# Performance work log

Measured on AMD Instinct MI355X. Metric: run time of the kernel, lower is better.

The kernel has to match this reference:

```python
import jax, jax.numpy as jnp
import numpy as np

T = 3          # num_node_type
B = 8          # batch
N = 512        # max_doc_len
F_IN = 256     # in_features
F_OUT = 128    # out_features
NE = 10        # num_edge_type (embedding has NE+1 rows, row 0 = padding)
ALPHA = 0.2    # leaky relu slope
NEG = -9e15    # masked-score fill, same constant as torch source


def setup_inputs() -> dict:
    key = jax.random.key(0)
    ks = jax.random.split(key, 7)
    node_rep = jax.random.normal(ks[0], (B, N, F_IN), jnp.float32)
    node_type_mask_rep = jax.random.uniform(ks[1], (T, B, N, 1), jnp.float32)
    adj = jax.random.randint(ks[2], (B, N, N), 0, NE + 1, jnp.int32)
    W = jax.random.normal(ks[3], (T, F_IN, F_OUT), jnp.float32) * 0.05
    b = jnp.zeros((T, F_OUT), jnp.float32)
    # attention vector a in R^{2F} split into halves (GAT trick): a([h_i, x2_ij]) = h_i.a1 + x2_ij.a2 + a_b
    a1 = jax.random.normal(ks[4], (F_OUT,), jnp.float32) * 0.05
    a2 = jax.random.normal(ks[5], (F_OUT,), jnp.float32) * 0.05
    a_b = jnp.zeros((), jnp.float32)
    emb = jax.random.normal(ks[6], (NE + 1, F_OUT), jnp.float32) * 0.05
    emb = emb.at[0].set(0.0)  # padding_idx=0
    return {"node_rep": node_rep, "node_type_mask_rep": node_type_mask_rep,
            "adj": adj, "W": W, "b": b, "a1": a1, "a2": a2, "a_b": a_b, "emb": emb}


def reference(node_rep, node_type_mask_rep, adj, W, b, a1, a2, a_b, emb):
    # typed projection: h = sum_t (node_rep @ W_t + b_t) * mask_t   -> (B, N, F_OUT)
    h = jnp.sum((jnp.einsum('bni,tio->tbno', node_rep, W) + b[:, None, None, :])
                * node_type_mask_rep, axis=0)
    # edge-type embeddings: (B, N, N, F_OUT)
    E = emb[adj]
    # x_2[b,i,j] = h[b,j] + E[b,i,j]
    x2 = h[:, None, :, :] + E
    # score[b,i,j] = leakyrelu(a1.h_i + a2.x2_ij + a_b)  (decomposed concat-linear)
    s = (jnp.einsum('bif,f->bi', h, a1)[:, :, None]
         + jnp.einsum('bijf,f->bij', x2, a2) + a_b)
    s = jnp.where(s > 0, s, ALPHA * s)
    s = jnp.where(adj > 0, s, jnp.float32(NEG))
    attn = jax.nn.softmax(s, axis=2)
    # weighted sum over neighbors of x_2 (NOT h), then ELU
    out = jnp.einsum('bij,bijf->bif', attn, x2)
    return jax.nn.elu(out)
```

## Files before the change

### kernel.cpp

```cpp
#include <hip/hip_runtime.h>

constexpr int kB    = 8;
constexpr int kN    = 512;
constexpr int kFIN  = 256;
constexpr int kFOUT = 128;
constexpr int kNE   = 10;
constexpr int kBN   = kB * kN;
constexpr float kALPHA = 0.2f;
constexpr float kNEG   = -9e15f;

typedef __attribute__((ext_vector_type(8))) short bhalf8;
typedef __attribute__((ext_vector_type(4))) float f32x4;

__device__ __forceinline__ unsigned short bf16_trunc(float x) {
    union { float f; unsigned u; } c; c.f = x;
    return (unsigned short)(c.u >> 16);
}
__device__ __forceinline__ float bf16_tof(unsigned short h) {
    union { unsigned u; float f; } c; c.u = ((unsigned)h) << 16;
    return c.f;
}

__global__ __launch_bounds__(256) void prep_kernel(
    const float* __restrict__ W,
    const float* __restrict__ emb,
    const float* __restrict__ a2,
    unsigned short* __restrict__ Whp,
    unsigned short* __restrict__ Wlp,
    float* __restrict__ emb_a2)
{
    const int tid = threadIdx.x;
    if (blockIdx.x < 48) {
        const int g    = blockIdx.x * 256 + tid;
        const int lane = g & 63;
        const int nt   = (g >> 6) & 7;
        const int ks   = (g >> 9) & 7;
        const int tt   = g >> 12;
        const int col  = nt * 16 + (lane & 15);
        const int kb   = ks * 32 + ((lane >> 4) * 8);
        unsigned short hbuf[8], lbuf[8];
        #pragma unroll
        for (int j = 0; j < 8; ++j) {
            const float w = W[((size_t)tt * kFIN + kb + j) * kFOUT + col];
            hbuf[j] = bf16_trunc(w);
            lbuf[j] = bf16_trunc(w - bf16_tof(hbuf[j]));
        }
        const size_t dst = ((size_t)((tt * 8 + ks) * 8 + nt)) * 512 + lane * 8;
        #pragma unroll
        for (int j = 0; j < 8; ++j) { Whp[dst + j] = hbuf[j]; Wlp[dst + j] = lbuf[j]; }
    } else if (tid < 176) {
        const int e = tid >> 4, l = tid & 15;
        float p = 0.f;
        #pragma unroll
        for (int k8 = 0; k8 < 8; ++k8)
            p += emb[e * kFOUT + l + k8 * 16] * a2[l + k8 * 16];
        #pragma unroll
        for (int off = 8; off; off >>= 1) p += __shfl_xor(p, off);
        if (l == 0) emb_a2[e] = p;
    }
}

__global__ __launch_bounds__(512) void proj_kernel(
    const float* __restrict__ node_rep,
    const float* __restrict__ mask,
    const float* __restrict__ bias,
    const unsigned short* __restrict__ Whp,
    const unsigned short* __restrict__ Wlp,
    const float* __restrict__ a1,
    const float* __restrict__ a2,
    const float* __restrict__ a_b,
    float* __restrict__ h,
    float* __restrict__ s1,
    float* __restrict__ s2)
{
    __shared__ short xsh[32][264];
    __shared__ short xsl[32][264];

    const int tid  = threadIdx.x;
    const int row0 = blockIdx.x * 32;

    #pragma unroll
    for (int it = 0; it < 4; ++it) {
        const int idx = tid + it * 512;
        const int r = idx >> 6, q = idx & 63;
        const float4 v = *(const float4*)&node_rep[(size_t)(row0 + r) * kFIN + q * 4];
        ushort4 hi, lo;
        hi.x = bf16_trunc(v.x); lo.x = bf16_trunc(v.x - bf16_tof(hi.x));
        hi.y = bf16_trunc(v.y); lo.y = bf16_trunc(v.y - bf16_tof(hi.y));
        hi.z = bf16_trunc(v.z); lo.z = bf16_trunc(v.z - bf16_tof(hi.z));
        hi.w = bf16_trunc(v.w); lo.w = bf16_trunc(v.w - bf16_tof(hi.w));
        *(ushort4*)&xsh[r][q * 4] = hi;
        *(ushort4*)&xsl[r][q * 4] = lo;
    }
    __syncthreads();

    const int wave = tid >> 6, lane = tid & 63;
    const int wrow = wave & 1, wcol = wave >> 1;
    const int arow = wrow * 16 + (lane & 15);
    const int koff = (lane >> 4) * 8;

    f32x4 acc[3][2];
    #pragma unroll
    for (int t = 0; t < 3; ++t)
        #pragma unroll
        for (int nt = 0; nt < 2; ++nt) acc[t][nt] = (f32x4){0,0,0,0};

    #pragma unroll 2
    for (int ks = 0; ks < 8; ++ks) {
        const bhalf8 Ah = *(const bhalf8*)&xsh[arow][ks * 32 + koff];
        const bhalf8 Al = *(const bhalf8*)&xsl[arow][ks * 32 + koff];
        #pragma unroll
        for (int t = 0; t < 3; ++t)
            #pragma unroll
            for (int nt = 0; nt < 2; ++nt) {
                const size_t bw =
                    ((size_t)((t * 8 + ks) * 8 + wcol * 2 + nt)) * 512 + lane * 8;
                const bhalf8 Bh = *(const bhalf8*)(Whp + bw);
                const bhalf8 Bl = *(const bhalf8*)(Wlp + bw);
                acc[t][nt] = __builtin_amdgcn_mfma_f32_16x16x32_bf16(Ah, Bh, acc[t][nt], 0, 0, 0);
                acc[t][nt] = __builtin_amdgcn_mfma_f32_16x16x32_bf16(Ah, Bl, acc[t][nt], 0, 0, 0);
                acc[t][nt] = __builtin_amdgcn_mfma_f32_16x16x32_bf16(Al, Bh, acc[t][nt], 0, 0, 0);
            }
    }
    __syncthreads();

    float* hstash = (float*)xsh;

    const int rA = wrow * 16 + ((lane >> 4) * 4);
    const int cA = lane & 15;
    #pragma unroll
    for (int j = 0; j < 4; ++j) {
        const int row = row0 + rA + j;
        const float m0 = mask[row];
        const float m1 = mask[kBN + row];
        const float m2 = mask[2 * kBN + row];
        #pragma unroll
        for (int nt = 0; nt < 2; ++nt) {
            const int col = wcol * 32 + nt * 16 + cA;
            const float hv = m0 * (acc[0][nt][j] + bias[col])
                           + m1 * (acc[1][nt][j] + bias[kFOUT + col])
                           + m2 * (acc[2][nt][j] + bias[2 * kFOUT + col]);
            h[(size_t)row * kFOUT + col] = hv;
            hstash[(rA + j) * 132 + col] = hv;
        }
    }
    __syncthreads();

    #pragma unroll
    for (int rr = 0; rr < 4; ++rr) {
        const int r = wave * 4 + rr;
        const float v0 = hstash[r * 132 + lane];
        const float v1 = hstash[r * 132 + 64 + lane];
        float p1 = v0 * a1[lane] + v1 * a1[64 + lane];
        float p2 = v0 * a2[lane] + v1 * a2[64 + lane];
        #pragma unroll
        for (int off = 32; off; off >>= 1) {
            p1 += __shfl_down(p1, off);
            p2 += __shfl_down(p2, off);
        }
        if (lane == 0) {
            s1[row0 + r] = p1 + a_b[0];
            s2[row0 + r] = p2;
        }
    }
}

__global__ __launch_bounds__(512) void attn_kernel(
    const int*   __restrict__ adj,
    const float* __restrict__ emb,
    const float* __restrict__ h,
    const float* __restrict__ s1,
    const float* __restrict__ s2,
    const float* __restrict__ emb_a2g,
    float* __restrict__ out)
{
    __shared__ float sc[8][kN + 4];
    __shared__ int   adjs[8][kN];
    __shared__ float scT[kN][8];
    __shared__ float wsum[8][16];
    __shared__ float ea2[16];

    const int tid = threadIdx.x;
    const int b   = blockIdx.x >> 6;
    const int i0  = (blockIdx.x & 63) * 8;

    if (tid < 16) ea2[tid] = emb_a2g[tid];
    __syncthreads();

    const int*   adjb = adj + ((size_t)(b * kN + i0)) * kN;
    const float* s2b  = s2 + b * kN;
    #pragma unroll
    for (int it = 0; it < 2; ++it) {
        const int idx = tid + it * 512;
        const int r = idx >> 7, jq = idx & 127;
        const int4   av  = *(const int4*)&adjb[(size_t)r * kN + jq * 4];
        const float4 s2v = *(const float4*)&s2b[jq * 4];
        const float  sr  = s1[b * kN + i0 + r];
        float4 sv; float s;
        s = sr + s2v.x + ea2[av.x]; s = s > 0.f ? s : kALPHA * s; sv.x = av.x > 0 ? s : kNEG;
        s = sr + s2v.y + ea2[av.y]; s = s > 0.f ? s : kALPHA * s; sv.y = av.y > 0 ? s : kNEG;
        s = sr + s2v.z + ea2[av.z]; s = s > 0.f ? s : kALPHA * s; sv.z = av.z > 0 ? s : kNEG;
        s = sr + s2v.w + ea2[av.w]; s = s > 0.f ? s : kALPHA * s; sv.w = av.w > 0 ? s : kNEG;
        *(float4*)&sc[r][jq * 4] = sv;
        *(int4*)&adjs[r][jq * 4] = av;
    }
    __syncthreads();

    {
        const int r = tid >> 6, lane = tid & 63;
        float v[8]; int av[8];
        #pragma unroll
        for (int k = 0; k < 8; ++k) {
            v[k]  = sc[r][lane + k * 64];
            av[k] = adjs[r][lane + k * 64];
        }
        float m = v[0];
        #pragma unroll
        for (int k = 1; k < 8; ++k) m = fmaxf(m, v[k]);
        #pragma unroll
        for (int off = 32; off; off >>= 1) m = fmaxf(m, __shfl_xor(m, off));
        float sum = 0.f;
        #pragma unroll
        for (int k = 0; k < 8; ++k) { v[k] = __expf(v[k] - m); sum += v[k]; }
        #pragma unroll
        for (int off = 32; off; off >>= 1) sum += __shfl_xor(sum, off);
        const float inv = 1.0f / sum;
        #pragma unroll
        for (int k = 0; k < 8; ++k) {
            v[k] *= inv;
            scT[lane + k * 64][r] = v[k];
        }
        #pragma unroll
        for (int e = 1; e <= kNE; ++e) {
            float p = 0.f;
            #pragma unroll
            for (int k = 0; k < 8; ++k) p += (av[k] == e) ? v[k] : 0.f;
            #pragma unroll
            for (int off = 32; off; off >>= 1) p += __shfl_xor(p, off);
            if (lane == 0) wsum[r][e] = p;
        }
    }
    __syncthreads();

    const int f4l = tid & 31;
    const int rg  = (tid >> 5) & 1;
    const int js  = tid >> 6;
    const float* hb  = h + ((size_t)(b * kN + js * 64)) * kFOUT + f4l * 4;
    const float* sct = &scT[js * 64][rg * 4];

    float4 acc0 = {0,0,0,0}, acc1 = {0,0,0,0}, acc2 = {0,0,0,0}, acc3 = {0,0,0,0};
    #pragma unroll 4
    for (int jj = 0; jj < 64; ++jj) {
        const float4 w4 = *(const float4*)&sct[jj * 8];
        const float4 hv = *(const float4*)&hb[(size_t)jj * kFOUT];
        acc0.x = fmaf(w4.x, hv.x, acc0.x); acc0.y = fmaf(w4.x, hv.y, acc0.y);
        acc0.z = fmaf(w4.x, hv.z, acc0.z); acc0.w = fmaf(w4.x, hv.w, acc0.w);
        acc1.x = fmaf(w4.y, hv.x, acc1.x); acc1.y = fmaf(w4.y, hv.y, acc1.y);
        acc1.z = fmaf(w4.y, hv.z, acc1.z); acc1.w = fmaf(w4.y, hv.w, acc1.w);
        acc2.x = fmaf(w4.z, hv.x, acc2.x); acc2.y = fmaf(w4.z, hv.y, acc2.y);
        acc2.z = fmaf(w4.z, hv.z, acc2.z); acc2.w = fmaf(w4.z, hv.w, acc2.w);
        acc3.x = fmaf(w4.w, hv.x, acc3.x); acc3.y = fmaf(w4.w, hv.y, acc3.y);
        acc3.z = fmaf(w4.w, hv.z, acc3.z); acc3.w = fmaf(w4.w, hv.w, acc3.w);
    }
    __syncthreads();

    float* parts_lo = (float*)adjs;
    float* parts_hi = (float*)sc;
    {
        float* pbase = (js < 4) ? parts_lo + js * 1024
                                : parts_hi + (js - 4) * 1024;
        const int rbase = rg * 4;
        *(float4*)&pbase[(rbase + 0) * kFOUT + f4l * 4] = acc0;
        *(float4*)&pbase[(rbase + 1) * kFOUT + f4l * 4] = acc1;
        *(float4*)&pbase[(rbase + 2) * kFOUT + f4l * 4] = acc2;
        *(float4*)&pbase[(rbase + 3) * kFOUT + f4l * 4] = acc3;
    }
    __syncthreads();

    if (tid < 256) {
        const int r  = tid >> 5;
        const int fl = (tid & 31) * 4;
        float4 a = {0,0,0,0};
        #pragma unroll
        for (int p = 0; p < 4; ++p) {
            const float4 v0 = *(const float4*)&parts_lo[p * 1024 + r * kFOUT + fl];
            const float4 v1 = *(const float4*)&parts_hi[p * 1024 + r * kFOUT + fl];
            a.x += v0.x + v1.x; a.y += v0.y + v1.y;
            a.z += v0.z + v1.z; a.w += v0.w + v1.w;
        }
        #pragma unroll
        for (int e = 1; e <= kNE; ++e) {
            const float  wv = wsum[r][e];
            const float4 ev = *(const float4*)&emb[e * kFOUT + fl];
            a.x = fmaf(wv, ev.x, a.x); a.y = fmaf(wv, ev.y, a.y);
            a.z = fmaf(wv, ev.z, a.z); a.w = fmaf(wv, ev.w, a.w);
        }
        a.x = a.x > 0.f ? a.x : expm1f(a.x);
        a.y = a.y > 0.f ? a.y : expm1f(a.y);
        a.z = a.z > 0.f ? a.z : expm1f(a.z);
        a.w = a.w > 0.f ? a.w : expm1f(a.w);
        *(float4*)&out[((size_t)(b * kN + i0 + r)) * kFOUT + fl] = a;
    }
}

extern "C" void kernel_launch(void* const* d_in, const int* in_sizes, int n_in,
                              void* d_out, int out_size, void* d_ws, size_t ws_size,
                              hipStream_t stream) {
    const float* node_rep = (const float*)d_in[0];
    const float* mask     = (const float*)d_in[1];
    const int*   adj      = (const int*)  d_in[2];
    const float* W        = (const float*)d_in[3];
    const float* bias     = (const float*)d_in[4];
    const float* a1       = (const float*)d_in[5];
    const float* a2       = (const float*)d_in[6];
    const float* a_b      = (const float*)d_in[7];
    const float* emb      = (const float*)d_in[8];
    float* out = (float*)d_out;

    float* fws    = (float*)d_ws;
    float* h      = fws;
    float* s1     = h + (size_t)kBN * kFOUT;
    float* s2     = s1 + kBN;
    float* emb_a2 = s2 + kBN;
    unsigned short* Whp = (unsigned short*)(emb_a2 + 64);
    unsigned short* Wlp = Whp + 3 * 8 * 8 * 512;

    prep_kernel<<<49, 256, 0, stream>>>(W, emb, a2, Whp, Wlp, emb_a2);
    proj_kernel<<<kBN / 32, 512, 0, stream>>>(
        node_rep, mask, bias, Whp, Wlp, a1, a2, a_b, h, s1, s2);
    attn_kernel<<<kBN / 8, 512, 0, stream>>>(
        adj, emb, h, s1, s2, emb_a2, out);
}
```

Before: 111.5 us.

## Fuse projection and attention kernels with a global flag barrier

Merges the projection and attention kernels into one persistent-style launch. The first 128 blocks compute h, s1 and s2, then increment a global atomic counter. Every block prefetches its adjacency tile into shared memory before spinning on that counter, so the adjacency load overlaps the projection and one launch gap disappears. The cost is a spin-wait grid barrier, which can deadlock if the 512 blocks are not all co-resident, plus the overhead of polling.

```diff
diff --git a/kernel.cpp b/kernel.cpp
--- a/kernel.cpp
+++ b/kernel.cpp
@@ -6,6 +6,7 @@
 constexpr int kFOUT = 128;
 constexpr int kNE   = 10;
 constexpr int kBN   = kB * kN;
+constexpr int kProd = 128;
 constexpr float kALPHA = 0.2f;
 constexpr float kNEG   = -9e15f;
 
@@ -27,7 +28,8 @@
     const float* __restrict__ a2,
     unsigned short* __restrict__ Whp,
     unsigned short* __restrict__ Wlp,
-    float* __restrict__ emb_a2)
+    float* __restrict__ emb_a2,
+    unsigned* __restrict__ flag)
 {
     const int tid = threadIdx.x;
     if (blockIdx.x < 48) {
@@ -48,19 +50,22 @@
         const size_t dst = ((size_t)((tt * 8 + ks) * 8 + nt)) * 512 + lane * 8;
         #pragma unroll
         for (int j = 0; j < 8; ++j) { Whp[dst + j] = hbuf[j]; Wlp[dst + j] = lbuf[j]; }
-    } else if (tid < 176) {
-        const int e = tid >> 4, l = tid & 15;
-        float p = 0.f;
-        #pragma unroll
-        for (int k8 = 0; k8 < 8; ++k8)
-            p += emb[e * kFOUT + l + k8 * 16] * a2[l + k8 * 16];
-        #pragma unroll
-        for (int off = 8; off; off >>= 1) p += __shfl_xor(p, off);
-        if (l == 0) emb_a2[e] = p;
-    }
-}
-
-__global__ __launch_bounds__(512) void proj_kernel(
+    } else {
+        if (tid < 176) {
+            const int e = tid >> 4, l = tid & 15;
+            float p = 0.f;
+            #pragma unroll
+            for (int k8 = 0; k8 < 8; ++k8)
+                p += emb[e * kFOUT + l + k8 * 16] * a2[l + k8 * 16];
+            #pragma unroll
+            for (int off = 8; off; off >>= 1) p += __shfl_xor(p, off);
+            if (l == 0) emb_a2[e] = p;
+        }
+        if (tid == 192) *flag = 0u;
+    }
+}
+
+__global__ __launch_bounds__(512) void fused_kernel(
     const float* __restrict__ node_rep,
     const float* __restrict__ mask,
     const float* __restrict__ bias,
@@ -69,150 +74,163 @@
     const float* __restrict__ a1,
     const float* __restrict__ a2,
     const float* __restrict__ a_b,
+    const int*   __restrict__ adj,
+    const float* __restrict__ emb,
+    const float* __restrict__ emb_a2g,
     float* __restrict__ h,
     float* __restrict__ s1,
-    float* __restrict__ s2)
-{
-    __shared__ short xsh[32][264];
-    __shared__ short xsl[32][264];
-
-    const int tid  = threadIdx.x;
-    const int row0 = blockIdx.x * 32;
-
-    #pragma unroll
-    for (int it = 0; it < 4; ++it) {
-        const int idx = tid + it * 512;
-        const int r = idx >> 6, q = idx & 63;
-        const float4 v = *(const float4*)&node_rep[(size_t)(row0 + r) * kFIN + q * 4];
-        ushort4 hi, lo;
-        hi.x = bf16_trunc(v.x); lo.x = bf16_trunc(v.x - bf16_tof(hi.x));
-        hi.y = bf16_trunc(v.y); lo.y = bf16_trunc(v.y - bf16_tof(hi.y));
-        hi.z = bf16_trunc(v.z); lo.z = bf16_trunc(v.z - bf16_tof(hi.z));
-        hi.w = bf16_trunc(v.w); lo.w = bf16_trunc(v.w - bf16_tof(hi.w));
-        *(ushort4*)&xsh[r][q * 4] = hi;
-        *(ushort4*)&xsl[r][q * 4] = lo;
-    }
-    __syncthreads();
-
-    const int wave = tid >> 6, lane = tid & 63;
-    const int wrow = wave & 1, wcol = wave >> 1;
-    const int arow = wrow * 16 + (lane & 15);
-    const int koff = (lane >> 4) * 8;
-
-    f32x4 acc[3][2];
-    #pragma unroll
-    for (int t = 0; t < 3; ++t)
-        #pragma unroll
-        for (int nt = 0; nt < 2; ++nt) acc[t][nt] = (f32x4){0,0,0,0};
-
-    #pragma unroll 2
-    for (int ks = 0; ks < 8; ++ks) {
-        const bhalf8 Ah = *(const bhalf8*)&xsh[arow][ks * 32 + koff];
-        const bhalf8 Al = *(const bhalf8*)&xsl[arow][ks * 32 + koff];
-        #pragma unroll
-        for (int t = 0; t < 3; ++t)
-            #pragma unroll
-            for (int nt = 0; nt < 2; ++nt) {
-                const size_t bw =
-                    ((size_t)((t * 8 + ks) * 8 + wcol * 2 + nt)) * 512 + lane * 8;
-                const bhalf8 Bh = *(const bhalf8*)(Whp + bw);
-                const bhalf8 Bl = *(const bhalf8*)(Wlp + bw);
-                acc[t][nt] = __builtin_amdgcn_mfma_f32_16x16x32_bf16(Ah, Bh, acc[t][nt], 0, 0, 0);
-                acc[t][nt] = __builtin_amdgcn_mfma_f32_16x16x32_bf16(Ah, Bl, acc[t][nt], 0, 0, 0);
-                acc[t][nt] = __builtin_amdgcn_mfma_f32_16x16x32_bf16(Al, Bh, acc[t][nt], 0, 0, 0);
-            }
-    }
-    __syncthreads();
-
-    float* hstash = (float*)xsh;
-
-    const int rA = wrow * 16 + ((lane >> 4) * 4);
-    const int cA = lane & 15;
-    #pragma unroll
-    for (int j = 0; j < 4; ++j) {
-        const int row = row0 + rA + j;
-        const float m0 = mask[row];
-        const float m1 = mask[kBN + row];
-        const float m2 = mask[2 * kBN + row];
-        #pragma unroll
-        for (int nt = 0; nt < 2; ++nt) {
-            const int col = wcol * 32 + nt * 16 + cA;
-            const float hv = m0 * (acc[0][nt][j] + bias[col])
-                           + m1 * (acc[1][nt][j] + bias[kFOUT + col])
-                           + m2 * (acc[2][nt][j] + bias[2 * kFOUT + col]);
-            h[(size_t)row * kFOUT + col] = hv;
-            hstash[(rA + j) * 132 + col] = hv;
-        }
-    }
-    __syncthreads();
-
-    #pragma unroll
-    for (int rr = 0; rr < 4; ++rr) {
-        const int r = wave * 4 + rr;
-        const float v0 = hstash[r * 132 + lane];
-        const float v1 = hstash[r * 132 + 64 + lane];
-        float p1 = v0 * a1[lane] + v1 * a1[64 + lane];
-        float p2 = v0 * a2[lane] + v1 * a2[64 + lane];
-        #pragma unroll
-        for (int off = 32; off; off >>= 1) {
-            p1 += __shfl_down(p1, off);
-            p2 += __shfl_down(p2, off);
-        }
-        if (lane == 0) {
-            s1[row0 + r] = p1 + a_b[0];
-            s2[row0 + r] = p2;
-        }
-    }
-}
-
-__global__ __launch_bounds__(512) void attn_kernel(
-    const int*   __restrict__ adj,
-    const float* __restrict__ emb,
-    const float* __restrict__ h,
-    const float* __restrict__ s1,
-    const float* __restrict__ s2,
-    const float* __restrict__ emb_a2g,
+    float* __restrict__ s2,
+    unsigned* __restrict__ flag,
     float* __restrict__ out)
 {
-    __shared__ float sc[8][kN + 4];
-    __shared__ int   adjs[8][kN];
-    __shared__ float scT[kN][8];
-    __shared__ float wsum[8][16];
-    __shared__ float ea2[16];
-
-    const int tid = threadIdx.x;
-    const int b   = blockIdx.x >> 6;
-    const int i0  = (blockIdx.x & 63) * 8;
-
-    if (tid < 16) ea2[tid] = emb_a2g[tid];
-    __syncthreads();
-
-    const int*   adjb = adj + ((size_t)(b * kN + i0)) * kN;
-    const float* s2b  = s2 + b * kN;
+    __shared__ __align__(16) char pool[49856];
+
+    const int tid  = threadIdx.x;
+    const int bid  = blockIdx.x;
+    const int wave = tid >> 6, lane = tid & 63;
+
+    if (bid < kProd) {
+        short* xsh = (short*)pool;
+        short* xsl = xsh + 32 * 264;
+        const int row0 = bid * 32;
+
+        #pragma unroll
+        for (int it = 0; it < 4; ++it) {
+            const int idx = tid + it * 512;
+            const int r = idx >> 6, q = idx & 63;
+            const float4 v = *(const float4*)&node_rep[(size_t)(row0 + r) * kFIN + q * 4];
+            ushort4 hi, lo;
+            hi.x = bf16_trunc(v.x); lo.x = bf16_trunc(v.x - bf16_tof(hi.x));
+            hi.y = bf16_trunc(v.y); lo.y = bf16_trunc(v.y - bf16_tof(hi.y));
+            hi.z = bf16_trunc(v.z); lo.z = bf16_trunc(v.z - bf16_tof(hi.z));
+            hi.w = bf16_trunc(v.w); lo.w = bf16_trunc(v.w - bf16_tof(hi.w));
+            *(ushort4*)&xsh[r * 264 + q * 4] = hi;
+            *(ushort4*)&xsl[r * 264 + q * 4] = lo;
+        }
+        __syncthreads();
+
+        const int wrow = wave & 1, wcol = wave >> 1;
+        const int arow = wrow * 16 + (lane & 15);
+        const int koff = (lane >> 4) * 8;
+
+        f32x4 acc[3][2];
+        #pragma unroll
+        for (int t = 0; t < 3; ++t)
+            #pragma unroll
+            for (int nt = 0; nt < 2; ++nt) acc[t][nt] = (f32x4){0, 0, 0, 0};
+
+        #pragma unroll 2
+        for (int ks = 0; ks < 8; ++ks) {
+            const bhalf8 Ah = *(const bhalf8*)&xsh[arow * 264 + ks * 32 + koff];
+            const bhalf8 Al = *(const bhalf8*)&xsl[arow * 264 + ks * 32 + koff];
+            #pragma unroll
+            for (int t = 0; t < 3; ++t)
+                #pragma unroll
+                for (int nt = 0; nt < 2; ++nt) {
+                    const size_t bw =
+                        ((size_t)((t * 8 + ks) * 8 + wcol * 2 + nt)) * 512 + lane * 8;
+                    const bhalf8 Bh = *(const bhalf8*)(Whp + bw);
+                    const bhalf8 Bl = *(const bhalf8*)(Wlp + bw);
+                    acc[t][nt] = __builtin_amdgcn_mfma_f32_16x16x32_bf16(Ah, Bh, acc[t][nt], 0, 0, 0);
+                    acc[t][nt] = __builtin_amdgcn_mfma_f32_16x16x32_bf16(Ah, Bl, acc[t][nt], 0, 0, 0);
+                    acc[t][nt] = __builtin_amdgcn_mfma_f32_16x16x32_bf16(Al, Bh, acc[t][nt], 0, 0, 0);
+                }
+        }
+        __syncthreads();
+
+        float* hstash = (float*)pool;
+        const int rA = wrow * 16 + ((lane >> 4) * 4);
+        const int cA = lane & 15;
+        #pragma unroll
+        for (int j = 0; j < 4; ++j) {
+            const int row = row0 + rA + j;
+            const float m0 = mask[row];
+            const float m1 = mask[kBN + row];
+            const float m2 = mask[2 * kBN + row];
+            #pragma unroll
+            for (int nt = 0; nt < 2; ++nt) {
+                const int col = wcol * 32 + nt * 16 + cA;
+                const float hv = m0 * (acc[0][nt][j] + bias[col])
+                               + m1 * (acc[1][nt][j] + bias[kFOUT + col])
+                               + m2 * (acc[2][nt][j] + bias[2 * kFOUT + col]);
+                h[(size_t)row * kFOUT + col] = hv;
+                hstash[(rA + j) * 132 + col] = hv;
+            }
+        }
+        __syncthreads();
+
+        #pragma unroll
+        for (int rr = 0; rr < 4; ++rr) {
+            const int r = wave * 4 + rr;
+            const float v0 = hstash[r * 132 + lane];
+            const float v1 = hstash[r * 132 + 64 + lane];
+            float p1 = v0 * a1[lane] + v1 * a1[64 + lane];
+            float p2 = v0 * a2[lane] + v1 * a2[64 + lane];
+            #pragma unroll
+            for (int off = 32; off; off >>= 1) {
+                p1 += __shfl_down(p1, off);
+                p2 += __shfl_down(p2, off);
+            }
+            if (lane == 0) {
+                s1[row0 + r] = p1 + a_b[0];
+                s2[row0 + r] = p2;
+            }
+        }
+        __syncthreads();
+        __threadfence();
+        if (tid == 0)
+            __hip_atomic_fetch_add(flag, 1u, __ATOMIC_RELEASE, __HIP_MEMORY_SCOPE_AGENT);
+    }
+
+    float* sc    = (float*)pool;
+    int*   adjs  = (int*)(pool + 16512);
+    float* scT   = (float*)(pool + 32896);
+    float* wsumS = (float*)(pool + 49280);
+    float* ea2s  = (float*)(pool + 49792);
+
+    const int b  = bid >> 6;
+    const int i0 = (bid & 63) * 8;
+
+    const int* adjb = adj + ((size_t)(b * kN + i0)) * kN;
     #pragma unroll
     for (int it = 0; it < 2; ++it) {
         const int idx = tid + it * 512;
         const int r = idx >> 7, jq = idx & 127;
-        const int4   av  = *(const int4*)&adjb[(size_t)r * kN + jq * 4];
+        *(int4*)&adjs[r * 512 + jq * 4] = *(const int4*)&adjb[(size_t)r * kN + jq * 4];
+    }
+    if (tid < 16) ea2s[tid] = emb_a2g[tid];
+
+    if (tid == 0) {
+        while (__hip_atomic_load(flag, __ATOMIC_ACQUIRE, __HIP_MEMORY_SCOPE_AGENT)
+               < (unsigned)kProd)
+            __builtin_amdgcn_s_sleep(8);
+    }
+    __syncthreads();
+
+    const float* s2b = s2 + b * kN;
+    #pragma unroll
+    for (int it = 0; it < 2; ++it) {
+        const int idx = tid + it * 512;
+        const int r = idx >> 7, jq = idx & 127;
+        const int4   av  = *(const int4*)&adjs[r * 512 + jq * 4];
         const float4 s2v = *(const float4*)&s2b[jq * 4];
         const float  sr  = s1[b * kN + i0 + r];
         float4 sv; float s;
-        s = sr + s2v.x + ea2[av.x]; s = s > 0.f ? s : kALPHA * s; sv.x = av.x > 0 ? s : kNEG;
-        s = sr + s2v.y + ea2[av.y]; s = s > 0.f ? s : kALPHA * s; sv.y = av.y > 0 ? s : kNEG;
-        s = sr + s2v.z + ea2[av.z]; s = s > 0.f ? s : kALPHA * s; sv.z = av.z > 0 ? s : kNEG;
-        s = sr + s2v.w + ea2[av.w]; s = s > 0.f ? s : kALPHA * s; sv.w = av.w > 0 ? s : kNEG;
-        *(float4*)&sc[r][jq * 4] = sv;
-        *(int4*)&adjs[r][jq * 4] = av;
+        s = sr + s2v.x + ea2s[av.x]; s = s > 0.f ? s : kALPHA * s; sv.x = av.x > 0 ? s : kNEG;
+        s = sr + s2v.y + ea2s[av.y]; s = s > 0.f ? s : kALPHA * s; sv.y = av.y > 0 ? s : kNEG;
+        s = sr + s2v.z + ea2s[av.z]; s = s > 0.f ? s : kALPHA * s; sv.z = av.z > 0 ? s : kNEG;
+        s = sr + s2v.w + ea2s[av.w]; s = s > 0.f ? s : kALPHA * s; sv.w = av.w > 0 ? s : kNEG;
+        *(float4*)&sc[r * 516 + jq * 4] = sv;
     }
     __syncthreads();
 
     {
-        const int r = tid >> 6, lane = tid & 63;
+        const int r = wave;
         float v[8]; int av[8];
         #pragma unroll
         for (int k = 0; k < 8; ++k) {
-            v[k]  = sc[r][lane + k * 64];
-            av[k] = adjs[r][lane + k * 64];
+            v[k]  = sc[r * 516 + lane + k * 64];
+            av[k] = adjs[r * 512 + lane + k * 64];
         }
         float m = v[0];
         #pragma unroll
@@ -228,7 +246,7 @@
         #pragma unroll
         for (int k = 0; k < 8; ++k) {
             v[k] *= inv;
-            scT[lane + k * 64][r] = v[k];
+            scT[(lane + k * 64) * 8 + r] = v[k];
         }
         #pragma unroll
         for (int e = 1; e <= kNE; ++e) {
@@ -237,7 +255,7 @@
             for (int k = 0; k < 8; ++k) p += (av[k] == e) ? v[k] : 0.f;
             #pragma unroll
             for (int off = 32; off; off >>= 1) p += __shfl_xor(p, off);
-            if (lane == 0) wsum[r][e] = p;
+            if (lane == 0) wsumS[r * 16 + e] = p;
         }
     }
     __syncthreads();
@@ -246,7 +264,7 @@
     const int rg  = (tid >> 5) & 1;
     const int js  = tid >> 6;
     const float* hb  = h + ((size_t)(b * kN + js * 64)) * kFOUT + f4l * 4;
-    const float* sct = &scT[js * 64][rg * 4];
+    const float* sct = &scT[(js * 64) * 8 + rg * 4];
 
     float4 acc0 = {0,0,0,0}, acc1 = {0,0,0,0}, acc2 = {0,0,0,0}, acc3 = {0,0,0,0};
     #pragma unroll 4
@@ -264,8 +282,8 @@
     }
     __syncthreads();
 
-    float* parts_lo = (float*)adjs;
-    float* parts_hi = (float*)sc;
+    float* parts_lo = (float*)(pool + 16512);
+    float* parts_hi = (float*)pool;
     {
         float* pbase = (js < 4) ? parts_lo + js * 1024
                                 : parts_hi + (js - 4) * 1024;
@@ -280,7 +298,7 @@
     if (tid < 256) {
         const int r  = tid >> 5;
         const int fl = (tid & 31) * 4;
-        float4 a = {0,0,0,0};
+        float4 a = {0, 0, 0, 0};
         #pragma unroll
         for (int p = 0; p < 4; ++p) {
             const float4 v0 = *(const float4*)&parts_lo[p * 1024 + r * kFOUT + fl];
@@ -290,7 +308,7 @@
         }
         #pragma unroll
         for (int e = 1; e <= kNE; ++e) {
-            const float  wv = wsum[r][e];
+            const float  wv = wsumS[r * 16 + e];
             const float4 ev = *(const float4*)&emb[e * kFOUT + fl];
             a.x = fmaf(wv, ev.x, a.x); a.y = fmaf(wv, ev.y, a.y);
             a.z = fmaf(wv, ev.z, a.z); a.w = fmaf(wv, ev.w, a.w);
@@ -322,12 +340,12 @@
     float* s1     = h + (size_t)kBN * kFOUT;
     float* s2     = s1 + kBN;
     float* emb_a2 = s2 + kBN;
-    unsigned short* Whp = (unsigned short*)(emb_a2 + 64);
+    unsigned* flag = (unsigned*)(emb_a2 + 64);
+    unsigned short* Whp = (unsigned short*)(flag + 16);
     unsigned short* Wlp = Whp + 3 * 8 * 8 * 512;
 
-    prep_kernel<<<49, 256, 0, stream>>>(W, emb, a2, Whp, Wlp, emb_a2);
-    proj_kernel<<<kBN / 32, 512, 0, stream>>>(
-        node_rep, mask, bias, Whp, Wlp, a1, a2, a_b, h, s1, s2);
-    attn_kernel<<<kBN / 8, 512, 0, stream>>>(
-        adj, emb, h, s1, s2, emb_a2, out);
-}
+    prep_kernel<<<49, 256, 0, stream>>>(W, emb, a2, Whp, Wlp, emb_a2, flag);
+    fused_kernel<<<512, 512, 0, stream>>>(
+        node_rep, mask, bias, Whp, Wlp, a1, a2, a_b, adj, emb, emb_a2,
+        h, s1, s2, flag, out);
+}
```

Result: slower. 256.5 us (+129.9%).
